# Optimization experiments

Hardware: AMD Instinct MI355X
Metric: run time of the kernel (lower is better)

Reference implementation:

```python
import jax, jax.numpy as jnp
import numpy as np

B, V, E, N = 4, 16384, 4, 32
F, U = 1024, 1024


def setup_inputs() -> dict:
    key = jax.random.key(0)
    k1, k2, k3 = jax.random.split(key, 3)
    # adjacency values in [-1, V); -1 marks non-existent neighbours
    adjacency = jax.random.randint(k1, (B, V, E, N), -1, V, dtype=jnp.int32)
    # force some vertices to be fully invalid (all -1) so the mask path matters
    invalid_vertex = jax.random.uniform(k2, (B, V, 1, 1)) < 0.25
    adjacency = jnp.where(invalid_vertex, jnp.int32(-1), adjacency)
    features = jax.random.normal(k3, (B, V, F), dtype=jnp.float32)
    kernel = jax.random.normal(jax.random.fold_in(key, 10), (F, U), dtype=jnp.float32) * (1.0 / np.sqrt(F))
    bias = jnp.zeros((U,), dtype=jnp.float32)
    return {"adjacency": adjacency, "features": features, "kernel": kernel, "bias": bias}


def reference(adjacency, features, kernel, bias):
    # A vertex is "valid" if it has at least one neighbour (any adjacency entry >= 0)
    valid = jnp.any(adjacency >= 0, axis=(2, 3))  # [B, V]
    # Dense per-node linear transform (1x1-conv analogue) + bias + relu
    out = jax.nn.relu(jnp.einsum('bvf,fu->bvu', features, kernel) + bias)  # [B, V, U]
    f_in, f_out = kernel.shape
    if f_in == f_out:
        def_features = features  # invalid vertices keep their input features
    else:
        def_features = jnp.zeros(features.shape[:-1] + (f_out,), dtype=features.dtype)
    # scatter transformed features back only at valid vertices
    return jnp.where(valid[..., None], out, def_features)
```

## Files before the change

### kernel.cpp

```cpp
#include <hip/hip_runtime.h>

#define MTOT 65536
#define KTOT 1024
#define NTOT 1024

#define BM 256
#define BN 256
#define BK 32
#define NSTEP (KTOT / BK)

typedef __attribute__((ext_vector_type(4))) unsigned int u32x4;
typedef __attribute__((ext_vector_type(4))) float f32x4;
typedef __attribute__((ext_vector_type(8))) __bf16 bf16x8;
typedef __attribute__((ext_vector_type(4))) unsigned short u16x4;

static __device__ __forceinline__ unsigned short f2bf(float f) {
    unsigned int u = __float_as_uint(f);
    u += 0x7fffu + ((u >> 16) & 1u);
    return (unsigned short)(u >> 16);
}

#define GLOAD16(g, l)                                                              \
    __builtin_amdgcn_global_load_lds(                                              \
        (const __attribute__((address_space(1))) void*)(g),                        \
        (__attribute__((address_space(3))) void*)(l), 16, 0, 0)

#define VMCNT(n) asm volatile("s_waitcnt vmcnt(" #n ")" ::: "memory")
#define CFENCE   asm volatile("" ::: "memory")
#define BAR()    __builtin_amdgcn_s_barrier()

__global__ __launch_bounds__(256) void prep_kernel(const int* __restrict__ adj,
                                                   const float* __restrict__ feat,
                                                   unsigned short* __restrict__ abf,
                                                   unsigned char* __restrict__ valid,
                                                   float* __restrict__ out) {
    const int row  = blockIdx.x * 4 + (threadIdx.x >> 6);
    const int lane = threadIdx.x & 63;
    const int2 a2  = reinterpret_cast<const int2*>(adj)[(size_t)row * 64 + lane];
    const bool anyv = __any((a2.x >= 0) || (a2.y >= 0)) != 0;

    const f32x4* frow = reinterpret_cast<const f32x4*>(feat + (size_t)row * KTOT);
    u16x4*       brow = reinterpret_cast<u16x4*>(abf + (size_t)row * KTOT);
    f32x4*       orow = reinterpret_cast<f32x4*>(out + (size_t)row * NTOT);
    if (anyv) {
#pragma unroll
        for (int i = 0; i < 4; ++i) {
            const f32x4 v = frow[lane + 64 * i];
            u16x4 b;
            b.x = f2bf(v[0]); b.y = f2bf(v[1]); b.z = f2bf(v[2]); b.w = f2bf(v[3]);
            brow[lane + 64 * i] = b;
        }
    } else {
#pragma unroll
        for (int i = 0; i < 4; ++i)
            orow[lane + 64 * i] = frow[lane + 64 * i];
    }
    if (lane == 0) valid[row] = anyv ? 1 : 0;
}

__global__ __launch_bounds__(256) void transposeB_kernel(const float* __restrict__ kern,
                                                         unsigned short* __restrict__ kT) {
    __shared__ float tile[32][33];
    const int bx = blockIdx.x & 31;
    const int by = blockIdx.x >> 5;
    const int tx = threadIdx.x & 31;
    const int ty = threadIdx.x >> 5;
#pragma unroll
    for (int r = 0; r < 4; ++r)
        tile[ty + r * 8][tx] = kern[(size_t)(by * 32 + ty + r * 8) * NTOT + bx * 32 + tx];
    __syncthreads();
#pragma unroll
    for (int r = 0; r < 4; ++r)
        kT[(size_t)(bx * 32 + ty + r * 8) * KTOT + by * 32 + tx] = f2bf(tile[tx][ty + r * 8]);
}

__global__ __launch_bounds__(1024, 4) void gemm_kernel(const unsigned short* __restrict__ A,
                                                       const unsigned short* __restrict__ Bt,
                                                       const float* __restrict__ bias,
                                                       const unsigned char* __restrict__ valid,
                                                       float* __restrict__ out) {
    __shared__ __align__(16) unsigned short Asm[4 * 8192];
    __shared__ __align__(16) unsigned short Bsm[4 * 8192];

    const int tid  = threadIdx.x;
    const int lane = tid & 63;
    const int wv   = tid >> 6;
    const int wm   = wv >> 2;
    const int wn   = wv & 3;

    const int cpx = (int)gridDim.x >> 3;
    const int swz = ((int)blockIdx.x & 7) * cpx + ((int)blockIdx.x >> 3);
    const int bm  = swz >> 2;
    const int bn  = swz & 3;
    const size_t m0 = (size_t)bm * BM;
    const int    n0 = bn * BN;

    const int srow   = tid >> 2;
    const int lch    = (tid & 3) ^ ((tid >> 3) & 3);
    const size_t s_goff = (size_t)srow * KTOT + lch * 8;
    const int    s_loff = wv << 9;

    const unsigned short* Agl = A  + m0 * (size_t)KTOT + s_goff;
    const unsigned short* Bgl = Bt + (size_t)n0 * KTOT + s_goff;

#define STAGE(b, kt) do {                                                          \
        GLOAD16(Agl + (kt) * BK, &Asm[(b) * 8192 + s_loff]);                       \
        GLOAD16(Bgl + (kt) * BK, &Bsm[(b) * 8192 + s_loff]);                       \
    } while (0)

    const int lr  = lane & 15;
    const int g4  = lane >> 4;
    const int rsw = (g4 ^ ((lr >> 1) & 3)) << 3;
    int aridx[4], bridx[4];
#pragma unroll
    for (int m = 0; m < 4; ++m)
        aridx[m] = (wm * 64 + m * 16 + lr) * BK + rsw;
#pragma unroll
    for (int n = 0; n < 4; ++n)
        bridx[n] = (wn * 64 + n * 16 + lr) * BK + rsw;

    f32x4 acc[4][4];
#pragma unroll
    for (int m = 0; m < 4; ++m)
#pragma unroll
        for (int n = 0; n < 4; ++n)
            acc[m][n] = {0.0f, 0.0f, 0.0f, 0.0f};

    STAGE(0, 0);
    STAGE(1, 1);
    STAGE(2, 2);
    VMCNT(4);
    BAR(); CFENCE;

#pragma unroll
    for (int t = 0; t < NSTEP; ++t) {
        if (t + 3 < NSTEP) STAGE((t + 3) & 3, t + 3);
        const int b = t & 3;
        bf16x8 af[4], bf[4];
#pragma unroll
        for (int n = 0; n < 4; ++n)
            bf[n] = __builtin_bit_cast(bf16x8, *reinterpret_cast<const u32x4*>(&Bsm[b * 8192 + bridx[n]]));
#pragma unroll
        for (int m = 0; m < 4; ++m)
            af[m] = __builtin_bit_cast(bf16x8, *reinterpret_cast<const u32x4*>(&Asm[b * 8192 + aridx[m]]));
        __builtin_amdgcn_s_setprio(1);
#pragma unroll
        for (int m = 0; m < 4; ++m)
#pragma unroll
            for (int n = 0; n < 4; ++n)
                acc[m][n] = __builtin_amdgcn_mfma_f32_16x16x32_bf16(af[m], bf[n], acc[m][n], 0, 0, 0);
        __builtin_amdgcn_s_setprio(0);
        if (t < NSTEP - 3)       VMCNT(4);
        else if (t == NSTEP - 3) VMCNT(2);
        else if (t == NSTEP - 2) VMCNT(0);
        if (t < NSTEP - 1) { BAR(); CFENCE; }
    }

    float bv[4];
#pragma unroll
    for (int n = 0; n < 4; ++n)
        bv[n] = bias[n0 + wn * 64 + n * 16 + lr];

#pragma unroll
    for (int m = 0; m < 4; ++m) {
#pragma unroll
        for (int q = 0; q < 4; ++q) {
            const size_t row = m0 + wm * 64 + m * 16 + g4 * 4 + q;
            if (valid[row]) {
                const size_t ro = row * NTOT + n0 + wn * 64 + lr;
#pragma unroll
                for (int n = 0; n < 4; ++n)
                    out[ro + n * 16] = fmaxf(acc[m][n][q] + bv[n], 0.0f);
            }
        }
    }
#undef STAGE
}

extern "C" void kernel_launch(void* const* d_in, const int* in_sizes, int n_in,
                              void* d_out, int out_size, void* d_ws, size_t ws_size,
                              hipStream_t stream) {
    const int*   adj  = (const int*)d_in[0];
    const float* feat = (const float*)d_in[1];
    const float* kern = (const float*)d_in[2];
    const float* bias = (const float*)d_in[3];
    float* out = (float*)d_out;

    unsigned short* kT    = (unsigned short*)d_ws;
    unsigned char*  valid = (unsigned char*)d_ws + 2 * 1024 * 1024;
    unsigned short* abf   = (unsigned short*)((char*)d_ws + 2 * 1024 * 1024 + 65536);

    transposeB_kernel<<<(KTOT / 32) * (NTOT / 32), 256, 0, stream>>>(kern, kT);
    prep_kernel<<<MTOT / 4, 256, 0, stream>>>(adj, feat, abf, valid, out);
    gemm_kernel<<<(MTOT / BM) * (NTOT / BN), 1024, 0, stream>>>(abf, kT, bias, valid, out);
}
```

Measured before the change: 261.1 us.

## Compact valid rows before GEMM to skip compute on invalid vertices

Adds a valid-count kernel, a single-block prefix scan and a compaction prep kernel, so that only valid rows are written densely into the bf16 A buffer along with a row index map. The GEMM then exits early for row tiles beyond the valid count and scatters its outputs through the index map. This avoids MFMA work on invalid rows, which the setup makes about a quarter of all rows. The cost is two extra launches, a second pass over the validity data and a scattered epilogue. A fallback to the old path remains for when the workspace is too small.

```diff
diff --git a/kernel.cpp b/kernel.cpp
--- a/kernel.cpp
+++ b/kernel.cpp
@@ -8,6 +8,7 @@
 #define BN 256
 #define BK 32
 #define NSTEP (KTOT / BK)
+#define NCHUNK 4096
 
 typedef __attribute__((ext_vector_type(4))) unsigned int u32x4;
 typedef __attribute__((ext_vector_type(4))) float f32x4;
@@ -29,33 +30,101 @@
 #define CFENCE   asm volatile("" ::: "memory")
 #define BAR()    __builtin_amdgcn_s_barrier()
 
-__global__ __launch_bounds__(256) void prep_kernel(const int* __restrict__ adj,
-                                                   const float* __restrict__ feat,
-                                                   unsigned short* __restrict__ abf,
-                                                   unsigned char* __restrict__ valid,
-                                                   float* __restrict__ out) {
-    const int row  = blockIdx.x * 4 + (threadIdx.x >> 6);
-    const int lane = threadIdx.x & 63;
-    const int2 a2  = reinterpret_cast<const int2*>(adj)[(size_t)row * 64 + lane];
-    const bool anyv = __any((a2.x >= 0) || (a2.y >= 0)) != 0;
-
-    const f32x4* frow = reinterpret_cast<const f32x4*>(feat + (size_t)row * KTOT);
-    u16x4*       brow = reinterpret_cast<u16x4*>(abf + (size_t)row * KTOT);
-    f32x4*       orow = reinterpret_cast<f32x4*>(out + (size_t)row * NTOT);
-    if (anyv) {
-#pragma unroll
-        for (int i = 0; i < 4; ++i) {
-            const f32x4 v = frow[lane + 64 * i];
-            u16x4 b;
-            b.x = f2bf(v[0]); b.y = f2bf(v[1]); b.z = f2bf(v[2]); b.w = f2bf(v[3]);
-            brow[lane + 64 * i] = b;
-        }
-    } else {
-#pragma unroll
-        for (int i = 0; i < 4; ++i)
-            orow[lane + 64 * i] = frow[lane + 64 * i];
-    }
-    if (lane == 0) valid[row] = anyv ? 1 : 0;
+__global__ __launch_bounds__(256) void valid_count_kernel(const int* __restrict__ adj,
+                                                          unsigned char* __restrict__ valid,
+                                                          int* __restrict__ chunkcnt) {
+    __shared__ int vb[16];
+    const int c    = blockIdx.x;
+    const int tid  = threadIdx.x;
+    const int wv   = tid >> 6;
+    const int lane = tid & 63;
+#pragma unroll
+    for (int r = 0; r < 4; ++r) {
+        const int row = c * 16 + wv * 4 + r;
+        const int2 a2 = reinterpret_cast<const int2*>(adj)[(size_t)row * 64 + lane];
+        const int anyv = __any((a2.x >= 0) || (a2.y >= 0));
+        if (lane == 0) { vb[wv * 4 + r] = anyv; valid[row] = (unsigned char)anyv; }
+    }
+    __syncthreads();
+    if (tid == 0) {
+        int s = 0;
+#pragma unroll
+        for (int i = 0; i < 16; ++i) s += vb[i];
+        chunkcnt[c] = s;
+    }
+}
+
+__global__ __launch_bounds__(1024) void scan_kernel(const int* __restrict__ chunkcnt,
+                                                    int* __restrict__ chunkoff,
+                                                    int* __restrict__ nv) {
+    __shared__ int sc[1024];
+    const int t = threadIdx.x;
+    const int b = t * 4;
+    const int c0 = chunkcnt[b], c1 = chunkcnt[b + 1], c2 = chunkcnt[b + 2], c3 = chunkcnt[b + 3];
+    const int s = c0 + c1 + c2 + c3;
+    sc[t] = s;
+    __syncthreads();
+    for (int d = 1; d < 1024; d <<= 1) {
+        const int v = (t >= d) ? sc[t - d] : 0;
+        __syncthreads();
+        sc[t] += v;
+        __syncthreads();
+    }
+    const int excl = sc[t] - s;
+    chunkoff[b]     = excl;
+    chunkoff[b + 1] = excl + c0;
+    chunkoff[b + 2] = excl + c0 + c1;
+    chunkoff[b + 3] = excl + c0 + c1 + c2;
+    if (t == 1023) nv[0] = sc[t];
+}
+
+__global__ __launch_bounds__(256) void prep_compact_kernel(const unsigned char* __restrict__ valid,
+                                                           const int* __restrict__ chunkoff,
+                                                           const float* __restrict__ feat,
+                                                           unsigned short* __restrict__ abf,
+                                                           int* __restrict__ cidx,
+                                                           float* __restrict__ out) {
+    __shared__ int cposL[16];
+    __shared__ int vL[16];
+    const int c    = blockIdx.x;
+    const int tid  = threadIdx.x;
+    const int wv   = tid >> 6;
+    const int lane = tid & 63;
+
+    if (tid < 64) {
+        const int v = (lane < 16) ? (int)valid[c * 16 + lane] : 0;
+        const unsigned long long mask = __ballot(v != 0);
+        if (lane < 16) {
+            const int pc = __popcll(mask & ((1ull << lane) - 1ull));
+            const int cp = chunkoff[c] + pc;
+            cposL[lane] = cp;
+            vL[lane]    = v;
+            if (v) cidx[cp] = c * 16 + lane;
+        }
+    }
+    __syncthreads();
+
+#pragma unroll
+    for (int r = 0; r < 4; ++r) {
+        const int li  = wv * 4 + r;
+        const int row = c * 16 + li;
+        const f32x4* frow = reinterpret_cast<const f32x4*>(feat + (size_t)row * KTOT);
+        if (vL[li]) {
+            u16x4* brow = reinterpret_cast<u16x4*>(abf + (size_t)cposL[li] * KTOT);
+#pragma unroll
+            for (int i = 0; i < 4; ++i) {
+                const f32x4 v = frow[lane + 64 * i];
+                u16x4 b;
+                b.x = f2bf(v[0]); b.y = f2bf(v[1]); b.z = f2bf(v[2]); b.w = f2bf(v[3]);
+                brow[lane + 64 * i] = b;
+            }
+        } else {
+            f32x4* orow = reinterpret_cast<f32x4*>(out + (size_t)row * NTOT);
+#pragma unroll
+            for (int i = 0; i < 4; ++i)
+                orow[lane + 64 * i] = frow[lane + 64 * i];
+        }
+    }
 }
 
 __global__ __launch_bounds__(256) void transposeB_kernel(const float* __restrict__ kern,
@@ -77,10 +146,13 @@
 __global__ __launch_bounds__(1024, 4) void gemm_kernel(const unsigned short* __restrict__ A,
                                                        const unsigned short* __restrict__ Bt,
                                                        const float* __restrict__ bias,
-                                                       const unsigned char* __restrict__ valid,
+                                                       const int* __restrict__ cidx,
+                                                       const int* __restrict__ nv,
                                                        float* __restrict__ out) {
     __shared__ __align__(16) unsigned short Asm[4 * 8192];
     __shared__ __align__(16) unsigned short Bsm[4 * 8192];
+
+    const int nvalid = nv[0];
 
     const int tid  = threadIdx.x;
     const int lane = tid & 63;
@@ -88,79 +160,193 @@
     const int wm   = wv >> 2;
     const int wn   = wv & 3;
 
+    const int cpx = (int)gridDim.x >> 3;
+    const int swz = ((int)blockIdx.x & 7) * cpx + ((int)blockIdx.x >> 3);
+    const int bm  = swz >> 2;
+    const int bn  = swz & 3;
+    const int m0i = bm * BM;
+    if (m0i >= nvalid) return;
+    const size_t m0 = (size_t)m0i;
+    const int    n0 = bn * BN;
+
+    const int srow   = tid >> 2;
+    const int lch    = (tid & 3) ^ ((tid >> 3) & 3);
+    const size_t s_goff = (size_t)srow * KTOT + lch * 8;
+    const int    s_loff = wv << 9;
+
+    const unsigned short* Agl = A  + m0 * (size_t)KTOT + s_goff;
+    const unsigned short* Bgl = Bt + (size_t)n0 * KTOT + s_goff;
+
+#define STAGE(b, kt) do {                                                          \
+        GLOAD16(Agl + (kt) * BK, &Asm[(b) * 8192 + s_loff]);                       \
+        GLOAD16(Bgl + (kt) * BK, &Bsm[(b) * 8192 + s_loff]);                       \
+    } while (0)
+
+    const int lr  = lane & 15;
+    const int g4  = lane >> 4;
+    const int rsw = (g4 ^ ((lr >> 1) & 3)) << 3;
+    int aridx[4], bridx[4];
+#pragma unroll
+    for (int m = 0; m < 4; ++m)
+        aridx[m] = (wm * 64 + m * 16 + lr) * BK + rsw;
+#pragma unroll
+    for (int n = 0; n < 4; ++n)
+        bridx[n] = (wn * 64 + n * 16 + lr) * BK + rsw;
+
+    f32x4 acc[4][4];
+#pragma unroll
+    for (int m = 0; m < 4; ++m)
+#pragma unroll
+        for (int n = 0; n < 4; ++n)
+            acc[m][n] = {0.0f, 0.0f, 0.0f, 0.0f};
+
+    STAGE(0, 0);
+    STAGE(1, 1);
+    STAGE(2, 2);
+    VMCNT(4);
+    BAR(); CFENCE;
+
+#pragma unroll
+    for (int t = 0; t < NSTEP; ++t) {
+        if (t + 3 < NSTEP) STAGE((t + 3) & 3, t + 3);
+        const int b = t & 3;
+        bf16x8 af[4], bfr[4];
+#pragma unroll
+        for (int n = 0; n < 4; ++n)
+            bfr[n] = __builtin_bit_cast(bf16x8, *reinterpret_cast<const u32x4*>(&Bsm[b * 8192 + bridx[n]]));
+#pragma unroll
+        for (int m = 0; m < 4; ++m)
+            af[m] = __builtin_bit_cast(bf16x8, *reinterpret_cast<const u32x4*>(&Asm[b * 8192 + aridx[m]]));
+        __builtin_amdgcn_s_setprio(1);
+#pragma unroll
+        for (int m = 0; m < 4; ++m)
+#pragma unroll
+            for (int n = 0; n < 4; ++n)
+                acc[m][n] = __builtin_amdgcn_mfma_f32_16x16x32_bf16(af[m], bfr[n], acc[m][n], 0, 0, 0);
+        __builtin_amdgcn_s_setprio(0);
+        if (t < NSTEP - 3)       VMCNT(4);
+        else if (t == NSTEP - 3) VMCNT(2);
+        else if (t == NSTEP - 2) VMCNT(0);
+        if (t < NSTEP - 1) { BAR(); CFENCE; }
+    }
+
+    float bv[4];
+#pragma unroll
+    for (int n = 0; n < 4; ++n)
+        bv[n] = bias[n0 + wn * 64 + n * 16 + lr];
+
+#pragma unroll
+    for (int m = 0; m < 4; ++m) {
+#pragma unroll
+        for (int q = 0; q < 4; ++q) {
+            const int cr = m0i + wm * 64 + m * 16 + g4 * 4 + q;
+            if (cr < nvalid) {
+                const int orow = cidx[cr];
+                const size_t ro = (size_t)orow * NTOT + n0 + wn * 64 + lr;
+#pragma unroll
+                for (int n = 0; n < 4; ++n)
+                    out[ro + n * 16] = fmaxf(acc[m][n][q] + bv[n], 0.0f);
+            }
+        }
+    }
+#undef STAGE
+}
+
+__global__ __launch_bounds__(256) void prep_full_kernel(const int* __restrict__ adj,
+                                                        const float* __restrict__ feat,
+                                                        unsigned short* __restrict__ abf,
+                                                        unsigned char* __restrict__ valid,
+                                                        float* __restrict__ out) {
+    const int row  = blockIdx.x * 4 + (threadIdx.x >> 6);
+    const int lane = threadIdx.x & 63;
+    const int2 a2  = reinterpret_cast<const int2*>(adj)[(size_t)row * 64 + lane];
+    const bool anyv = __any((a2.x >= 0) || (a2.y >= 0)) != 0;
+    const f32x4* frow = reinterpret_cast<const f32x4*>(feat + (size_t)row * KTOT);
+    u16x4*       brow = reinterpret_cast<u16x4*>(abf + (size_t)row * KTOT);
+    f32x4*       orow = reinterpret_cast<f32x4*>(out + (size_t)row * NTOT);
+    if (anyv) {
+#pragma unroll
+        for (int i = 0; i < 4; ++i) {
+            const f32x4 v = frow[lane + 64 * i];
+            u16x4 b;
+            b.x = f2bf(v[0]); b.y = f2bf(v[1]); b.z = f2bf(v[2]); b.w = f2bf(v[3]);
+            brow[lane + 64 * i] = b;
+        }
+    } else {
+#pragma unroll
+        for (int i = 0; i < 4; ++i)
+            orow[lane + 64 * i] = frow[lane + 64 * i];
+    }
+    if (lane == 0) valid[row] = anyv ? 1 : 0;
+}
+
+__global__ __launch_bounds__(1024, 4) void gemm_full_kernel(const unsigned short* __restrict__ A,
+                                                            const unsigned short* __restrict__ Bt,
+                                                            const float* __restrict__ bias,
+                                                            const unsigned char* __restrict__ valid,
+                                                            float* __restrict__ out) {
+    __shared__ __align__(16) unsigned short Asm[4 * 8192];
+    __shared__ __align__(16) unsigned short Bsm[4 * 8192];
+    const int tid  = threadIdx.x;
+    const int lane = tid & 63;
+    const int wv   = tid >> 6;
+    const int wm   = wv >> 2;
+    const int wn   = wv & 3;
     const int cpx = (int)gridDim.x >> 3;
     const int swz = ((int)blockIdx.x & 7) * cpx + ((int)blockIdx.x >> 3);
     const int bm  = swz >> 2;
     const int bn  = swz & 3;
     const size_t m0 = (size_t)bm * BM;
     const int    n0 = bn * BN;
-
     const int srow   = tid >> 2;
     const int lch    = (tid & 3) ^ ((tid >> 3) & 3);
     const size_t s_goff = (size_t)srow * KTOT + lch * 8;
     const int    s_loff = wv << 9;
-
     const unsigned short* Agl = A  + m0 * (size_t)KTOT + s_goff;
     const unsigned short* Bgl = Bt + (size_t)n0 * KTOT + s_goff;
-
 #define STAGE(b, kt) do {                                                          \
         GLOAD16(Agl + (kt) * BK, &Asm[(b) * 8192 + s_loff]);                       \
         GLOAD16(Bgl + (kt) * BK, &Bsm[(b) * 8192 + s_loff]);                       \
     } while (0)
-
     const int lr  = lane & 15;
     const int g4  = lane >> 4;
     const int rsw = (g4 ^ ((lr >> 1) & 3)) << 3;
     int aridx[4], bridx[4];
 #pragma unroll
+    for (int m = 0; m < 4; ++m) aridx[m] = (wm * 64 + m * 16 + lr) * BK + rsw;
+#pragma unroll
+    for (int n = 0; n < 4; ++n) bridx[n] = (wn * 64 + n * 16 + lr) * BK + rsw;
+    f32x4 acc[4][4];
+#pragma unroll
     for (int m = 0; m < 4; ++m)
-        aridx[m] = (wm * 64 + m * 16 + lr) * BK + rsw;
-#pragma unroll
-    for (int n = 0; n < 4; ++n)
-        bridx[n] = (wn * 64 + n * 16 + lr) * BK + rsw;
-
-    f32x4 acc[4][4];
-#pragma unroll
-    for (int m = 0; m < 4; ++m)
-#pragma unroll
-        for (int n = 0; n < 4; ++n)
-            acc[m][n] = {0.0f, 0.0f, 0.0f, 0.0f};
-
-    STAGE(0, 0);
-    STAGE(1, 1);
-    STAGE(2, 2);
-    VMCNT(4);
-    BAR(); CFENCE;
-
+#pragma unroll
+        for (int n = 0; n < 4; ++n) acc[m][n] = {0.f, 0.f, 0.f, 0.f};
+    STAGE(0, 0); STAGE(1, 1); STAGE(2, 2);
+    VMCNT(4); BAR(); CFENCE;
 #pragma unroll
     for (int t = 0; t < NSTEP; ++t) {
         if (t + 3 < NSTEP) STAGE((t + 3) & 3, t + 3);
         const int b = t & 3;
-        bf16x8 af[4], bf[4];
+        bf16x8 af[4], bfr[4];
 #pragma unroll
         for (int n = 0; n < 4; ++n)
-            bf[n] = __builtin_bit_cast(bf16x8, *reinterpret_cast<const u32x4*>(&Bsm[b * 8192 + bridx[n]]));
+            bfr[n] = __builtin_bit_cast(bf16x8, *reinterpret_cast<const u32x4*>(&Bsm[b * 8192 + bridx[n]]));
 #pragma unroll
         for (int m = 0; m < 4; ++m)
             af[m] = __builtin_bit_cast(bf16x8, *reinterpret_cast<const u32x4*>(&Asm[b * 8192 + aridx[m]]));
-        __builtin_amdgcn_s_setprio(1);
 #pragma unroll
         for (int m = 0; m < 4; ++m)
 #pragma unroll
             for (int n = 0; n < 4; ++n)
-                acc[m][n] = __builtin_amdgcn_mfma_f32_16x16x32_bf16(af[m], bf[n], acc[m][n], 0, 0, 0);
-        __builtin_amdgcn_s_setprio(0);
+                acc[m][n] = __builtin_amdgcn_mfma_f32_16x16x32_bf16(af[m], bfr[n], acc[m][n], 0, 0, 0);
         if (t < NSTEP - 3)       VMCNT(4);
         else if (t == NSTEP - 3) VMCNT(2);
         else if (t == NSTEP - 2) VMCNT(0);
         if (t < NSTEP - 1) { BAR(); CFENCE; }
     }
-
     float bv[4];
 #pragma unroll
-    for (int n = 0; n < 4; ++n)
-        bv[n] = bias[n0 + wn * 64 + n * 16 + lr];
-
+    for (int n = 0; n < 4; ++n) bv[n] = bias[n0 + wn * 64 + n * 16 + lr];
 #pragma unroll
     for (int m = 0; m < 4; ++m) {
 #pragma unroll
@@ -186,11 +372,26 @@
     const float* bias = (const float*)d_in[3];
     float* out = (float*)d_out;
 
-    unsigned short* kT    = (unsigned short*)d_ws;
-    unsigned char*  valid = (unsigned char*)d_ws + 2 * 1024 * 1024;
-    unsigned short* abf   = (unsigned short*)((char*)d_ws + 2 * 1024 * 1024 + 65536);
+    char* ws = (char*)d_ws;
+    unsigned short* kT    = (unsigned short*)ws;
+    unsigned char*  valid = (unsigned char*)(ws + (2u << 20));
+    int*  cidx     = (int*)(ws + (2u << 20) + (64u << 10));
+    int*  chunkcnt = (int*)(ws + (2u << 20) + (320u << 10));
+    int*  chunkoff = (int*)(ws + (2u << 20) + (336u << 10));
+    int*  nv       = (int*)(ws + (2u << 20) + (352u << 10));
+    unsigned short* abf = (unsigned short*)(ws + (4u << 20));
+
+    const size_t need = (4ull << 20) + (size_t)MTOT * KTOT * 2;
 
     transposeB_kernel<<<(KTOT / 32) * (NTOT / 32), 256, 0, stream>>>(kern, kT);
-    prep_kernel<<<MTOT / 4, 256, 0, stream>>>(adj, feat, abf, valid, out);
-    gemm_kernel<<<(MTOT / BM) * (NTOT / BN), 1024, 0, stream>>>(abf, kT, bias, valid, out);
-}
+    if (ws_size >= need) {
+        valid_count_kernel<<<NCHUNK, 256, 0, stream>>>(adj, valid, chunkcnt);
+        scan_kernel<<<1, 1024, 0, stream>>>(chunkcnt, chunkoff, nv);
+        prep_compact_kernel<<<NCHUNK, 256, 0, stream>>>(valid, chunkoff, feat, abf, cidx, out);
+        gemm_kernel<<<(MTOT / BM) * (NTOT / BN), 1024, 0, stream>>>(abf, kT, bias, cidx, nv, out);
+    } else {
+        unsigned short* abf_fb = (unsigned short*)(ws + (2u << 20) + (64u << 10));
+        prep_full_kernel<<<MTOT / 4, 256, 0, stream>>>(adj, feat, abf_fb, valid, out);
+        gemm_full_kernel<<<(MTOT / BM) * (NTOT / BN), 1024, 0, stream>>>(abf_fb, kT, bias, valid, out);
+    }
+}
```

After: 277.2 us. 1.06x slower.
